# Kernel tuning notes

Measured on AMD Instinct MI355X. Metric: run time of the kernel, lower is better.

## Reference

```python
import jax, jax.numpy as jnp
import numpy as np

B, N, C, H, NH, NC = 4, 2048, 256, 128, 8, 3  # batch, points, in_ch, hidden, heads, classes
DH = H // NH


def setup_inputs() -> dict:
    key = jax.random.key(0)
    ki = iter(jax.random.split(key, 48))
    def w(shape, s=0.05):
        return jax.random.normal(next(ki), shape, jnp.float32) * s
    z = lambda n: jnp.zeros((n,), jnp.float32)
    o = lambda n: jnp.ones((n,), jnp.float32)
    inp = dict(x=jax.random.normal(next(ki), (B, N, C), jnp.float32))
    inp.update(fuse_w1=w((H, C)), fuse_b1=z(H), fuse_w2=w((H, H)), fuse_b2=z(H))
    for l in range(2):
        inp[f'attn{l}_in_w'] = w((3 * H, H)); inp[f'attn{l}_in_b'] = z(3 * H)
        inp[f'attn{l}_out_w'] = w((H, H)); inp[f'attn{l}_out_b'] = z(H)
        inp[f'ffn{l}_w1'] = w((2 * H, H)); inp[f'ffn{l}_b1'] = z(2 * H)
        inp[f'ffn{l}_w2'] = w((H, 2 * H)); inp[f'ffn{l}_b2'] = z(H)
        inp[f'ln{2*l}_g'] = o(H); inp[f'ln{2*l}_b'] = z(H)
        inp[f'ln{2*l+1}_g'] = o(H); inp[f'ln{2*l+1}_b'] = z(H)
    inp.update(out_w1=w((H, H)), out_b1=z(H), out_w2=w((NC, H)), out_b2=z(NC))
    inp.update(det_w1=w((H // 2, H)), det_b1=z(H // 2), det_w2=w((1, H // 2)), det_b2=z(1))
    return inp


def _ln(x, g, b):
    m = jnp.mean(x, axis=-1, keepdims=True)
    v = jnp.mean((x - m) ** 2, axis=-1, keepdims=True)
    return (x - m) * jax.lax.rsqrt(v + 1e-5) * g + b


def _mha(x, in_w, in_b, out_w, out_b):
    # nn.MultiheadAttention (batch_first, self-attn), eval mode (no dropout)
    Bq, Nq, _ = x.shape
    qkv = x @ in_w.T + in_b                          # [B,N,3H]
    q, k, v = jnp.split(qkv, 3, axis=-1)
    q = q.reshape(Bq, Nq, NH, DH)
    k = k.reshape(Bq, Nq, NH, DH)
    v = v.reshape(Bq, Nq, NH, DH)
    s = jnp.einsum('bqhd,bkhd->bhqk', q, k) / jnp.sqrt(jnp.float32(DH))
    a = jax.nn.softmax(s, axis=-1)
    o = jnp.einsum('bhqk,bkhd->bqhd', a, v).reshape(Bq, Nq, H)
    return o @ out_w.T + out_b


def _forward(x, fuse_w1, fuse_b1, fuse_w2, fuse_b2,
             attn0_in_w, attn0_in_b, attn0_out_w, attn0_out_b,
             ffn0_w1, ffn0_b1, ffn0_w2, ffn0_b2, ln0_g, ln0_b, ln1_g, ln1_b,
             attn1_in_w, attn1_in_b, attn1_out_w, attn1_out_b,
             ffn1_w1, ffn1_b1, ffn1_w2, ffn1_b2, ln2_g, ln2_b, ln3_g, ln3_b,
             out_w1, out_b1, out_w2, out_b2, det_w1, det_b1, det_w2, det_b2):
    # feature_fusion (dropout = identity in eval)
    h = jnp.maximum(x @ fuse_w1.T + fuse_b1, 0) @ fuse_w2.T + fuse_b2
    layers = [
        (attn0_in_w, attn0_in_b, attn0_out_w, attn0_out_b, ffn0_w1, ffn0_b1, ffn0_w2, ffn0_b2, ln0_g, ln0_b, ln1_g, ln1_b),
        (attn1_in_w, attn1_in_b, attn1_out_w, attn1_out_b, ffn1_w1, ffn1_b1, ffn1_w2, ffn1_b2, ln2_g, ln2_b, ln3_g, ln3_b),
    ]
    for (iw, ib, ow, ob, f1w, f1b, f2w, f2b, g1, be1, g2, be2) in layers:
        h = _ln(h + _mha(h, iw, ib, ow, ob), g1, be1)
        h = _ln(h + (jnp.maximum(h @ f1w.T + f1b, 0) @ f2w.T + f2b), g2, be2)
    refined_logits = jnp.maximum(h @ out_w1.T + out_b1, 0) @ out_w2.T + out_b2   # [B,N,NC]
    head_prob = jax.nn.sigmoid(jnp.maximum(h @ det_w1.T + det_b1, 0) @ det_w2.T + det_b2)[..., 0]  # [B,N]
    quality = jnp.mean(head_prob, axis=1)                                        # [B]
    return refined_logits, head_prob, quality


def reference(x, fuse_w1, fuse_b1, fuse_w2, fuse_b2,
              attn0_in_w, attn0_in_b, attn0_out_w, attn0_out_b,
              ffn0_w1, ffn0_b1, ffn0_w2, ffn0_b2, ln0_g, ln0_b, ln1_g, ln1_b,
              attn1_in_w, attn1_in_b, attn1_out_w, attn1_out_b,
              ffn1_w1, ffn1_b1, ffn1_w2, ffn1_b2, ln2_g, ln2_b, ln3_g, ln3_b,
              out_w1, out_b1, out_w2, out_b2, det_w1, det_b1, det_w2, det_b2):
    return _forward(x, fuse_w1, fuse_b1, fuse_w2, fuse_b2,
                    attn0_in_w, attn0_in_b, attn0_out_w, attn0_out_b,
                    ffn0_w1, ffn0_b1, ffn0_w2, ffn0_b2, ln0_g, ln0_b, ln1_g, ln1_b,
                    attn1_in_w, attn1_in_b, attn1_out_w, attn1_out_b,
                    ffn1_w1, ffn1_b1, ffn1_w2, ffn1_b2, ln2_g, ln2_b, ln3_g, ln3_b,
                    out_w1, out_b1, out_w2, out_b2, det_w1, det_b1, det_w2, det_b2)
```

## Files before the change

### kernel.cpp

```cpp
#include <hip/hip_runtime.h>
#include <cstddef>

constexpr int Bb  = 4;
constexpr int Nn  = 2048;
constexpr int Cc  = 256;
constexpr int Hh  = 128;
constexpr int NHh = 8;
constexpr int DHh = 16;
constexpr int MTOK = Bb * Nn;
#define LOG2E 1.4426950408889634f

typedef __attribute__((ext_vector_type(8))) short bf16x8;
typedef __attribute__((ext_vector_type(4))) short bf16x4;
typedef __attribute__((ext_vector_type(4))) float f32x4;

__device__ __forceinline__ short f32_to_bf16_rne(float f) {
    union { float f; unsigned int u; } c; c.f = f;
    unsigned int r = c.u + 0x7fffu + ((c.u >> 16) & 1u);
    return (short)(r >> 16);
}
__device__ __forceinline__ float bf16_to_f32(short s) {
    union { float f; unsigned int u; } c; c.u = ((unsigned int)(unsigned short)s) << 16;
    return c.f;
}
__device__ __forceinline__ unsigned pack2_bf16(float a, float b) {
    unsigned r;
    asm("v_cvt_pk_bf16_f32 %0, %1, %2" : "=v"(r) : "v"(a), "v"(b));
    return r;
}

struct CvtJobs {
    const float* src[13];
    short*       dst[13];
    int          off[14];
    float*       qzero;
};

__global__ __launch_bounds__(256) void cvt_kernel(CvtJobs j) {
    const int gid = blockIdx.x * 256 + threadIdx.x;
    if (blockIdx.x == 0 && threadIdx.x < 4) j.qzero[threadIdx.x] = 0.f;
    if (gid >= j.off[13]) return;
    int k = 0;
    #pragma unroll
    for (int i = 0; i < 12; ++i) if (gid >= j.off[i + 1]) k = i + 1;
    const int idx = (gid - j.off[k]) * 4;
    float4 v = *(const float4*)(j.src[k] + idx);
    short o4[4] = { f32_to_bf16_rne(v.x), f32_to_bf16_rne(v.y),
                    f32_to_bf16_rne(v.z), f32_to_bf16_rne(v.w) };
    *(bf16x4*)(j.dst[k] + idx) = *(bf16x4*)o4;
}

__global__ __launch_bounds__(256) void qkv_gemm_kernel(
    const short* __restrict__ X, const short* __restrict__ W,
    const float* __restrict__ bias, short* __restrict__ Yb)
{
    constexpr int K = 128, N = 384, ST = K + 8;
    __shared__ short As[64 * ST];
    __shared__ short Bs[64 * ST];

    const int tid  = threadIdx.x;
    const int lane = tid & 63;
    const int wv   = tid >> 6;
    const int col  = lane & 15;
    const int g    = lane >> 4;
    const int m0   = blockIdx.y * 64;
    const int n0   = blockIdx.x * 64;

    for (int i = tid; i < 64 * (K / 8); i += 256) {
        const int r = i / (K / 8), c = (i % (K / 8)) * 8;
        *(bf16x8*)&As[r * ST + c] = *(const bf16x8*)(X + (size_t)(m0 + r) * K + c);
        *(bf16x8*)&Bs[r * ST + c] = *(const bf16x8*)(W + (size_t)(n0 + r) * K + c);
    }
    __syncthreads();

    f32x4 acc[4] = {};
    #pragma unroll
    for (int k0 = 0; k0 < K; k0 += 32) {
        bf16x8 a = *(bf16x8*)&As[(wv * 16 + col) * ST + k0 + g * 8];
        #pragma unroll
        for (int jj = 0; jj < 4; ++jj) {
            bf16x8 b = *(bf16x8*)&Bs[(jj * 16 + col) * ST + k0 + g * 8];
            acc[jj] = __builtin_amdgcn_mfma_f32_16x16x32_bf16(a, b, acc[jj], 0, 0, 0);
        }
    }

    #pragma unroll
    for (int jj = 0; jj < 4; ++jj) {
        const int cn = n0 + jj * 16 + col;
        const float bb = bias[cn];
        #pragma unroll
        for (int r = 0; r < 4; ++r) {
            const int rm = m0 + wv * 16 + g * 4 + r;
            Yb[(size_t)rm * N + cn] = f32_to_bf16_rne(acc[jj][r] + bb);
        }
    }
}

__global__ __launch_bounds__(256) void postattn_kernel(
    const short* __restrict__ X,
    const short* __restrict__ Wo, const float* __restrict__ bo,
    const short* __restrict__ W1, const float* __restrict__ b1,
    const short* __restrict__ W2, const float* __restrict__ b2,
    float* __restrict__ hf, short* __restrict__ hb,
    const float* __restrict__ g1w, const float* __restrict__ b1w,
    const float* __restrict__ g2w, const float* __restrict__ b2w)
{
    __shared__ short As[16 * 136];
    __shared__ short Ws[64 * 136];
    __shared__ short U1[16 * 136];
    __shared__ short U2[16 * 264];
    float* P = (float*)Ws;

    const int tid  = threadIdx.x;
    const int lane = tid & 63;
    const int wv   = tid >> 6;
    const int col  = lane & 15;
    const int g    = lane >> 4;
    const int m0   = blockIdx.x * 16;
    const int cb   = wv * 16;

    bf16x8 wreg[4];
    auto loadPanel = [&](const short* base, int stride) {
        #pragma unroll
        for (int j = 0; j < 4; ++j) {
            const int i = tid + j * 256;
            wreg[j] = *(const bf16x8*)(base + (size_t)(i / 16) * stride + (i % 16) * 8);
        }
    };
    auto writePanel = [&]() {
        #pragma unroll
        for (int j = 0; j < 4; ++j) {
            const int i = tid + j * 256;
            *(bf16x8*)&Ws[(i / 16) * 136 + (i % 16) * 8] = wreg[j];
        }
    };

    {
        const int r = tid / 16, c = (tid % 16) * 8;
        *(bf16x8*)&As[r * 136 + c] = *(const bf16x8*)(X + (size_t)(m0 + r) * 128 + c);
    }
    loadPanel(Wo, 128);

    f32x4 ya[2] = {};
    #pragma unroll
    for (int ch = 0; ch < 2; ++ch) {
        writePanel();
        if (ch == 0) loadPanel(Wo + (size_t)64 * 128, 128);
        else         loadPanel(W1, 128);
        asm volatile("s_waitcnt lgkmcnt(0)" ::: "memory");
        __builtin_amdgcn_s_barrier();
        #pragma unroll
        for (int k0 = 0; k0 < 128; k0 += 32) {
            bf16x8 a = *(bf16x8*)&As[col * 136 + k0 + g * 8];
            bf16x8 b = *(bf16x8*)&Ws[(cb + col) * 136 + k0 + g * 8];
            ya[ch] = __builtin_amdgcn_mfma_f32_16x16x32_bf16(a, b, ya[ch], 0, 0, 0);
        }
        __syncthreads();
    }

    #pragma unroll
    for (int ch = 0; ch < 2; ++ch) {
        const int cn = ch * 64 + cb + col;
        const float bb = bo[cn];
        #pragma unroll
        for (int r = 0; r < 4; ++r)
            P[(g * 4 + r) * 130 + cn] = ya[ch][r] + bb;
    }
    __syncthreads();

    float2 resid[4];
    #pragma unroll
    for (int rr = 0; rr < 4; ++rr) {
        const int row = wv * 4 + rr;
        const size_t t = m0 + row;
        float2 pv = *(float2*)&P[row * 130 + 2 * lane];
        float2 hv = ((const float2*)(hf + t * Hh))[lane];
        float a0 = hv.x + pv.x, a1 = hv.y + pv.y;
        float sum = a0 + a1;
        #pragma unroll
        for (int off = 32; off > 0; off >>= 1) sum += __shfl_xor(sum, off);
        const float mean = sum * (1.f / 128.f);
        const float d0 = a0 - mean, d1 = a1 - mean;
        float vs = d0 * d0 + d1 * d1;
        #pragma unroll
        for (int off = 32; off > 0; off >>= 1) vs += __shfl_xor(vs, off);
        const float rstd = rsqrtf(vs * (1.f / 128.f) + 1e-5f);
        float2 gv = ((const float2*)g1w)[lane];
        float2 bv = ((const float2*)b1w)[lane];
        float2 r = { d0 * rstd * gv.x + bv.x, d1 * rstd * gv.y + bv.y };
        resid[rr] = r;
        *(unsigned*)&U1[row * 136 + 2 * lane] = pack2_bf16(r.x, r.y);
    }
    __syncthreads();

    #pragma unroll
    for (int ch = 0; ch < 4; ++ch) {
        writePanel();
        if (ch < 3) loadPanel(W1 + (size_t)(ch + 1) * 64 * 128, 128);
        else        loadPanel(W2, 256);
        asm volatile("s_waitcnt lgkmcnt(0)" ::: "memory");
        __builtin_amdgcn_s_barrier();
        f32x4 y1 = {};
        #pragma unroll
        for (int k0 = 0; k0 < 128; k0 += 32) {
            bf16x8 a = *(bf16x8*)&U1[col * 136 + k0 + g * 8];
            bf16x8 b = *(bf16x8*)&Ws[(cb + col) * 136 + k0 + g * 8];
            y1 = __builtin_amdgcn_mfma_f32_16x16x32_bf16(a, b, y1, 0, 0, 0);
        }
        __syncthreads();
        const int cn = ch * 64 + cb + col;
        const float bb = b1[cn];
        #pragma unroll
        for (int r = 0; r < 4; ++r)
            U2[(g * 4 + r) * 264 + cn] = f32_to_bf16_rne(fmaxf(y1[r] + bb, 0.f));
    }

    f32x4 yb[2] = {};
    #pragma unroll
    for (int ch2 = 0; ch2 < 2; ++ch2) {
        #pragma unroll
        for (int kh = 0; kh < 2; ++kh) {
            writePanel();
            const int pidx = ch2 * 2 + kh;
            if (pidx < 3) {
                const int nj = pidx + 1;
                loadPanel(W2 + (size_t)(nj >> 1) * 64 * 256 + (nj & 1) * 128, 256);
            }
            asm volatile("s_waitcnt lgkmcnt(0)" ::: "memory");
            __builtin_amdgcn_s_barrier();
            #pragma unroll
            for (int k0 = 0; k0 < 128; k0 += 32) {
                bf16x8 a = *(bf16x8*)&U2[col * 264 + kh * 128 + k0 + g * 8];
                bf16x8 b = *(bf16x8*)&Ws[(cb + col) * 136 + k0 + g * 8];
                yb[ch2] = __builtin_amdgcn_mfma_f32_16x16x32_bf16(a, b, yb[ch2], 0, 0, 0);
            }
            __syncthreads();
        }
    }

    #pragma unroll
    for (int ch2 = 0; ch2 < 2; ++ch2) {
        const int cn = ch2 * 64 + cb + col;
        const float bb = b2[cn];
        #pragma unroll
        for (int r = 0; r < 4; ++r)
            P[(g * 4 + r) * 130 + cn] = yb[ch2][r] + bb;
    }
    __syncthreads();

    #pragma unroll
    for (int rr = 0; rr < 4; ++rr) {
        const int row = wv * 4 + rr;
        const size_t t = m0 + row;
        float2 pv = *(float2*)&P[row * 130 + 2 * lane];
        float a0 = resid[rr].x + pv.x, a1 = resid[rr].y + pv.y;
        float sum = a0 + a1;
        #pragma unroll
        for (int off = 32; off > 0; off >>= 1) sum += __shfl_xor(sum, off);
        const float mean = sum * (1.f / 128.f);
        const float d0 = a0 - mean, d1 = a1 - mean;
        float vs = d0 * d0 + d1 * d1;
        #pragma unroll
        for (int off = 32; off > 0; off >>= 1) vs += __shfl_xor(vs, off);
        const float rstd = rsqrtf(vs * (1.f / 128.f) + 1e-5f);
        float2 gv = ((const float2*)g2w)[lane];
        float2 bv = ((const float2*)b2w)[lane];
        float2 r = { d0 * rstd * gv.x + bv.x, d1 * rstd * gv.y + bv.y };
        ((float2*)(hf + t * Hh))[lane] = r;
        *(unsigned*)&hb[t * Hh + lane * 2] = pack2_bf16(r.x, r.y);
    }
}

template<int K, int MID, bool DO_LN>
__global__ __launch_bounds__(256) void mlp2_kernel(
    const short* __restrict__ X,
    const short* __restrict__ W1, const float* __restrict__ b1,
    const short* __restrict__ W2, const float* __restrict__ b2,
    float* __restrict__ hf, short* __restrict__ hb,
    const float* __restrict__ gw, const float* __restrict__ bw)
{
    constexpr int STA = K + 8;
    constexpr int STU = MID + 8;
    constexpr int KP1  = K / 128;
    constexpr int KP2  = MID / 128;
    constexpr int NCH1 = MID / 64;
    constexpr int NP1  = NCH1 * KP1;
    constexpr int NP   = NP1 + 2 * KP2;
    __shared__ short As[16 * STA];
    __shared__ short Ws[64 * 136];
    __shared__ short U[16 * STU];
    float* P = (float*)Ws;

    const int tid  = threadIdx.x;
    const int lane = tid & 63;
    const int wv   = tid >> 6;
    const int col  = lane & 15;
    const int g    = lane >> 4;
    const int m0   = blockIdx.x * 16;
    const int cb   = wv * 16;

    bf16x8 wreg[4];
    auto loadPanelIdx = [&](int idx) {
        const short* base;
        int stride;
        if (idx < NP1) {
            const int ch = idx / KP1, kh = idx % KP1;
            base = W1 + (size_t)(ch * 64) * K + kh * 128; stride = K;
        } else {
            const int jj = idx - NP1;
            const int ch2 = jj / KP2, kh = jj % KP2;
            base = W2 + (size_t)(ch2 * 64) * MID + kh * 128; stride = MID;
        }
        #pragma unroll
        for (int j = 0; j < 4; ++j) {
            const int i = tid + j * 256;
            wreg[j] = *(const bf16x8*)(base + (size_t)(i / 16) * stride + (i % 16) * 8);
        }
    };
    auto writePanel = [&]() {
        #pragma unroll
        for (int j = 0; j < 4; ++j) {
            const int i = tid + j * 256;
            *(bf16x8*)&Ws[(i / 16) * 136 + (i % 16) * 8] = wreg[j];
        }
    };

    for (int i = tid; i < 16 * (K / 8); i += 256) {
        const int r = i / (K / 8), c = (i % (K / 8)) * 8;
        *(bf16x8*)&As[r * STA + c] = *(const bf16x8*)(X + (size_t)(m0 + r) * K + c);
    }
    loadPanelIdx(0);
    int pidx = 0;

    #pragma unroll
    for (int ch = 0; ch < NCH1; ++ch) {
        f32x4 ya = {};
        #pragma unroll
        for (int kh = 0; kh < KP1; ++kh) {
            writePanel();
            ++pidx;
            if (pidx < NP) loadPanelIdx(pidx);
            asm volatile("s_waitcnt lgkmcnt(0)" ::: "memory");
            __builtin_amdgcn_s_barrier();
            #pragma unroll
            for (int k0 = 0; k0 < 128; k0 += 32) {
                bf16x8 a = *(bf16x8*)&As[col * STA + kh * 128 + k0 + g * 8];
                bf16x8 b = *(bf16x8*)&Ws[(cb + col) * 136 + k0 + g * 8];
                ya = __builtin_amdgcn_mfma_f32_16x16x32_bf16(a, b, ya, 0, 0, 0);
            }
            __syncthreads();
        }
        const int cn = ch * 64 + cb + col;
        const float bb = b1[cn];
        #pragma unroll
        for (int r = 0; r < 4; ++r)
            U[(g * 4 + r) * STU + cn] = f32_to_bf16_rne(fmaxf(ya[r] + bb, 0.f));
    }

    f32x4 yb[2] = {};
    #pragma unroll
    for (int ch2 = 0; ch2 < 2; ++ch2) {
        #pragma unroll
        for (int kh = 0; kh < KP2; ++kh) {
            writePanel();
            ++pidx;
            if (pidx < NP) loadPanelIdx(pidx);
            asm volatile("s_waitcnt lgkmcnt(0)" ::: "memory");
            __builtin_amdgcn_s_barrier();
            #pragma unroll
            for (int k0 = 0; k0 < 128; k0 += 32) {
                bf16x8 a = *(bf16x8*)&U[col * STU + kh * 128 + k0 + g * 8];
                bf16x8 b = *(bf16x8*)&Ws[(cb + col) * 136 + k0 + g * 8];
                yb[ch2] = __builtin_amdgcn_mfma_f32_16x16x32_bf16(a, b, yb[ch2], 0, 0, 0);
            }
            __syncthreads();
        }
    }

    #pragma unroll
    for (int ch2 = 0; ch2 < 2; ++ch2) {
        const int cn = ch2 * 64 + cb + col;
        const float bb = b2[cn];
        #pragma unroll
        for (int r = 0; r < 4; ++r)
            P[(g * 4 + r) * 130 + cn] = yb[ch2][r] + bb;
    }
    __syncthreads();

    #pragma unroll
    for (int rr = 0; rr < 4; ++rr) {
        const int row = wv * 4 + rr;
        const size_t t = m0 + row;
        float2 pv = *(float2*)&P[row * 130 + 2 * lane];
        if (DO_LN) {
            float2 hv = ((const float2*)(hf + t * Hh))[lane];
            float a0 = hv.x + pv.x, a1 = hv.y + pv.y;
            float sum = a0 + a1;
            #pragma unroll
            for (int off = 32; off > 0; off >>= 1) sum += __shfl_xor(sum, off);
            const float mean = sum * (1.f / 128.f);
            const float d0 = a0 - mean, d1 = a1 - mean;
            float vs = d0 * d0 + d1 * d1;
            #pragma unroll
            for (int off = 32; off > 0; off >>= 1) vs += __shfl_xor(vs, off);
            const float rstd = rsqrtf(vs * (1.f / 128.f) + 1e-5f);
            float2 gv = ((const float2*)gw)[lane];
            float2 bv = ((const float2*)bw)[lane];
            float2 r = { d0 * rstd * gv.x + bv.x, d1 * rstd * gv.y + bv.y };
            ((float2*)(hf + t * Hh))[lane] = r;
            *(unsigned*)&hb[t * Hh + lane * 2] = pack2_bf16(r.x, r.y);
        } else {
            ((float2*)(hf + t * Hh))[lane] = pv;
            *(unsigned*)&hb[t * Hh + lane * 2] = pack2_bf16(pv.x, pv.y);
        }
    }
}

__global__ __launch_bounds__(256) void head_kernel(
    const short* __restrict__ X,
    const short* __restrict__ W1b, const float* __restrict__ b1,
    const short* __restrict__ DW1b, const float* __restrict__ db1,
    const float* __restrict__ w2, const float* __restrict__ b2,
    const float* __restrict__ dw2, const float* __restrict__ db2,
    float* __restrict__ out)
{
    constexpr int K = 128, ST = K + 8;
    __shared__ short As[32 * ST];
    __shared__ short Ws[64 * ST];
    __shared__ float P[32 * 196];

    const int tid  = threadIdx.x;
    const int lane = tid & 63;
    const int wv   = tid >> 6;
    const int col  = lane & 15;
    const int g    = lane >> 4;
    const int m0   = blockIdx.x * 32;
    const int mst  = (wv & 1) * 16;
    const int cb   = (wv >> 1) * 32;

    bf16x8 wreg[4];
    auto loadPanel = [&](const short* base) {
        #pragma unroll
        for (int j = 0; j < 4; ++j) {
            const int i = tid + j * 256;
            wreg[j] = *(const bf16x8*)(base + (size_t)(i / 16) * K + (i % 16) * 8);
        }
    };
    auto writePanel = [&]() {
        #pragma unroll
        for (int j = 0; j < 4; ++j) {
            const int i = tid + j * 256;
            *(bf16x8*)&Ws[(i / 16) * ST + (i % 16) * 8] = wreg[j];
        }
    };

    for (int i = tid; i < 32 * (K / 8); i += 256) {
        const int r = i / (K / 8), c = (i % (K / 8)) * 8;
        *(bf16x8*)&As[r * ST + c] = *(const bf16x8*)(X + (size_t)(m0 + r) * K + c);
    }
    loadPanel(W1b);

    f32x4 ya[3][2] = {};
    #pragma unroll
    for (int ch = 0; ch < 3; ++ch) {
        writePanel();
        if (ch == 0) loadPanel(W1b + (size_t)64 * K);
        else if (ch == 1) loadPanel(DW1b);
        asm volatile("s_waitcnt lgkmcnt(0)" ::: "memory");
        __builtin_amdgcn_s_barrier();
        #pragma unroll
        for (int k0 = 0; k0 < K; k0 += 32) {
            bf16x8 a = *(bf16x8*)&As[(mst + col) * ST + k0 + g * 8];
            #pragma unroll
            for (int f = 0; f < 2; ++f) {
                bf16x8 b = *(bf16x8*)&Ws[(cb + f * 16 + col) * ST + k0 + g * 8];
                ya[ch][f] = __builtin_amdgcn_mfma_f32_16x16x32_bf16(a, b, ya[ch][f], 0, 0, 0);
            }
        }
        __syncthreads();
    }

    #pragma unroll
    for (int ch = 0; ch < 3; ++ch)
        #pragma unroll
        for (int f = 0; f < 2; ++f) {
            const int cn = ch * 64 + cb + f * 16 + col;
            const float bb = (cn < 128) ? b1[cn] : db1[cn - 128];
            #pragma unroll
            for (int r = 0; r < 4; ++r)
                P[(mst + g * 4 + r) * 196 + cn] = fmaxf(ya[ch][f][r] + bb, 0.f);
        }
    __syncthreads();

    const float w20 = w2[2 * lane],       w21 = w2[2 * lane + 1];
    const float w22 = w2[128 + 2 * lane], w23 = w2[129 + 2 * lane];
    const float w24 = w2[256 + 2 * lane], w25 = w2[257 + 2 * lane];
    const float dwl = dw2[lane];
    float qacc = 0.f;
    #pragma unroll
    for (int rr = 0; rr < 8; ++rr) {
        const int row = wv * 8 + rr;
        const size_t t = m0 + row;
        const float x0 = P[row * 196 + 2 * lane];
        const float x1 = P[row * 196 + 2 * lane + 1];
        float s0 = x0 * w20 + x1 * w21;
        float s1 = x0 * w22 + x1 * w23;
        float s2 = x0 * w24 + x1 * w25;
        float d  = P[row * 196 + 128 + lane] * dwl;
        #pragma unroll
        for (int off = 32; off > 0; off >>= 1) {
            s0 += __shfl_xor(s0, off);
            s1 += __shfl_xor(s1, off);
            s2 += __shfl_xor(s2, off);
            d  += __shfl_xor(d,  off);
        }
        if (lane == 0) {
            out[t * 3 + 0] = s0 + b2[0];
            out[t * 3 + 1] = s1 + b2[1];
            out[t * 3 + 2] = s2 + b2[2];
            const float prob = 1.f / (1.f + __expf(-(d + db2[0])));
            out[24576 + t] = prob;
            qacc += prob;
        }
    }
    if (lane == 0)
        atomicAdd(&out[32768 + (m0 >> 11)], qacc * (1.f / (float)Nn));
}

constexpr int KT = 128;
constexpr int KS = 28;
constexpr int VS = 132;

__global__ __launch_bounds__(256) void attn_kernel(
    const short* __restrict__ qkv, short* __restrict__ out)
{
    __shared__ short Ks[KT * KS];
    __shared__ short Vs[DHh * VS];

    const int tid  = threadIdx.x;
    const int lane = tid & 63;
    const int wv   = tid >> 6;
    const int col  = lane & 15;
    const int g    = lane >> 4;
    const int hd   = blockIdx.y;
    const int b    = blockIdx.z;
    const int q0   = blockIdx.x * 64 + wv * 16;

    const short* base = qkv + (size_t)b * Nn * 384;

    bf16x8 qf = {};
    if (g < 2) {
        bf16x8 qraw = *(const bf16x8*)(base + (size_t)(q0 + col) * 384 + hd * DHh + g * 8);
        const float qs = 0.25f * LOG2E;
        #pragma unroll
        for (int i = 0; i < 8; ++i)
            qf[i] = f32_to_bf16_rne(bf16_to_f32(qraw[i]) * qs);
    }

    f32x4 o    = {0.f, 0.f, 0.f, 0.f};
    f32x4 lacc = {0.f, 0.f, 0.f, 0.f};
    const short one_bf16 = (short)0x3F80;
    const bf16x8 ones = { one_bf16, one_bf16, one_bf16, one_bf16,
                          one_bf16, one_bf16, one_bf16, one_bf16 };

    const int ksr = tid >> 1;
    const int ksd = (tid & 1) * 8;
    const int va  = tid >> 2;
    const int vd  = (tid & 3) * 4;

    const short* kptr = base + (size_t)ksr * 384 + Hh + hd * DHh + ksd;
    const short* vptr = base + (size_t)(2 * va) * 384 + 2 * Hh + hd * DHh + vd;
    bf16x8 kreg = *(const bf16x8*)kptr;
    bf16x4 vr0  = *(const bf16x4*)vptr;
    bf16x4 vr1  = *(const bf16x4*)(vptr + 384);

    for (int kt = 0; kt < Nn; kt += KT) {
        __syncthreads();

        *(bf16x8*)&Ks[ksr * KS + ksd] = kreg;
        {
            unsigned a0 = ((const unsigned*)&vr0)[0], a1 = ((const unsigned*)&vr0)[1];
            unsigned b0 = ((const unsigned*)&vr1)[0], b1 = ((const unsigned*)&vr1)[1];
            *(unsigned*)&Vs[(vd + 0) * VS + 2 * va] = __builtin_amdgcn_perm(b0, a0, 0x05040100);
            *(unsigned*)&Vs[(vd + 1) * VS + 2 * va] = __builtin_amdgcn_perm(b0, a0, 0x07060302);
            *(unsigned*)&Vs[(vd + 2) * VS + 2 * va] = __builtin_amdgcn_perm(b1, a1, 0x05040100);
            *(unsigned*)&Vs[(vd + 3) * VS + 2 * va] = __builtin_amdgcn_perm(b1, a1, 0x07060302);
        }

        if (kt + KT < Nn) {
            kptr += KT * 384;
            vptr += KT * 384;
            kreg = *(const bf16x8*)kptr;
            vr0  = *(const bf16x4*)vptr;
            vr1  = *(const bf16x4*)(vptr + 384);
        }

        asm volatile("s_waitcnt lgkmcnt(0)" ::: "memory");
        __builtin_amdgcn_s_barrier();

        __builtin_amdgcn_s_setprio(1);
        #pragma unroll
        for (int s = 0; s < 4; ++s) {
            bf16x8 kf0 = {}, kf1 = {};
            if (g < 2) {
                kf0 = *(bf16x8*)&Ks[(s * 32 + col) * KS + g * 8];
                kf1 = *(bf16x8*)&Ks[(s * 32 + 16 + col) * KS + g * 8];
            }
            f32x4 z = {0.f, 0.f, 0.f, 0.f};
            f32x4 sA = __builtin_amdgcn_mfma_f32_16x16x32_bf16(kf0, qf, z, 0, 0, 0);
            f32x4 sB = __builtin_amdgcn_mfma_f32_16x16x32_bf16(kf1, qf, z, 0, 0, 0);

            union { bf16x8 v; unsigned u[4]; } pf;
            pf.u[0] = pack2_bf16(__builtin_amdgcn_exp2f(sA[0]),
                                 __builtin_amdgcn_exp2f(sA[1]));
            pf.u[1] = pack2_bf16(__builtin_amdgcn_exp2f(sA[2]),
                                 __builtin_amdgcn_exp2f(sA[3]));
            pf.u[2] = pack2_bf16(__builtin_amdgcn_exp2f(sB[0]),
                                 __builtin_amdgcn_exp2f(sB[1]));
            pf.u[3] = pack2_bf16(__builtin_amdgcn_exp2f(sB[2]),
                                 __builtin_amdgcn_exp2f(sB[3]));

            bf16x8 vf;
            ((bf16x4*)&vf)[0] = *(bf16x4*)&Vs[col * VS + s * 32 + g * 4];
            ((bf16x4*)&vf)[1] = *(bf16x4*)&Vs[col * VS + s * 32 + 16 + g * 4];

            o    = __builtin_amdgcn_mfma_f32_16x16x32_bf16(pf.v, vf,   o,    0, 0, 0);
            lacc = __builtin_amdgcn_mfma_f32_16x16x32_bf16(pf.v, ones, lacc, 0, 0, 0);
        }
        __builtin_amdgcn_s_setprio(0);
    }

    #pragma unroll
    for (int r = 0; r < 4; ++r) {
        const float inv = __builtin_amdgcn_rcpf(lacc[r]);
        out[(size_t)(b * Nn + q0 + g * 4 + r) * Hh + hd * DHh + col] =
            f32_to_bf16_rne(o[r] * inv);
    }
}

extern "C" void kernel_launch(void* const* d_in, const int* in_sizes, int n_in,
                              void* d_out, int out_size, void* d_ws, size_t ws_size,
                              hipStream_t stream)
{
    char* W8 = (char*)d_ws;
    float* hf   = (float*)(W8 + 0);
    short* hb   = (short*)(W8 + 4194304);
    short* wb   = (short*)(W8 + 6291456);
    char*  regA = W8 + 7340032;
    char*  regB = W8 + 13631488;

    short* xb    = (short*)regA;
    short* qkvb  = (short*)regA;
    short* attno = (short*)regB;
    float* out   = (float*)d_out;

    const int wsz[12]  = {32768,16384,49152,16384,32768,32768,49152,16384,32768,32768,16384,8192};
    const int wsrc[12] = {1, 3, 5, 7, 9, 11, 17, 19, 21, 23, 29, 33};
    int woff[13]; woff[0] = 0;
    for (int i = 0; i < 12; ++i) woff[i + 1] = woff[i] + wsz[i];

    CvtJobs jobs;
    int acc = 0;
    for (int i = 0; i < 12; ++i) {
        jobs.src[i] = (const float*)d_in[wsrc[i]];
        jobs.dst[i] = wb + woff[i];
        jobs.off[i] = acc;
        acc += wsz[i] / 4;
    }
    jobs.src[12] = (const float*)d_in[0];
    jobs.dst[12] = xb;
    jobs.off[12] = acc;
    acc += (MTOK * Cc) / 4;
    jobs.off[13] = acc;
    jobs.qzero = out + 32768;

    hipLaunchKernelGGL(cvt_kernel, dim3((acc + 255) / 256), dim3(256), 0, stream, jobs);

    hipLaunchKernelGGL((mlp2_kernel<256, 128, false>), dim3(MTOK / 16), dim3(256), 0,
                       stream, xb, wb + woff[0], (const float*)d_in[2],
                       wb + woff[1], (const float*)d_in[4], hf, hb, nullptr, nullptr);

    for (int l = 0; l < 2; ++l) {
        const int ib = 5 + l * 12;
        const int wbase = 2 + l * 4;
        hipLaunchKernelGGL(qkv_gemm_kernel, dim3(384 / 64, MTOK / 64), dim3(256), 0, stream,
                           hb, wb + woff[wbase + 0], (const float*)d_in[ib + 1], qkvb);
        hipLaunchKernelGGL(attn_kernel, dim3(Nn / 64, NHh, Bb), dim3(256), 0, stream,
                           qkvb, attno);
        hipLaunchKernelGGL(postattn_kernel, dim3(MTOK / 16), dim3(256), 0, stream,
                           attno, wb + woff[wbase + 1], (const float*)d_in[ib + 3],
                           wb + woff[wbase + 2], (const float*)d_in[ib + 5],
                           wb + woff[wbase + 3], (const float*)d_in[ib + 7],
                           hf, hb,
                           (const float*)d_in[ib + 8], (const float*)d_in[ib + 9],
                           (const float*)d_in[ib + 10], (const float*)d_in[ib + 11]);
    }

    hipLaunchKernelGGL(head_kernel, dim3(MTOK / 32), dim3(256), 0, stream,
                       hb, wb + woff[10], (const float*)d_in[30],
                       wb + woff[11], (const float*)d_in[34],
                       (const float*)d_in[31], (const float*)d_in[32],
                       (const float*)d_in[35], (const float*)d_in[36], out);
}
```

Before: 254.5 us.

## Double-buffer LDS weight and K/V tiles to drop one barrier per stage

Weight panels in postattn and mlp2 and the K/V tiles in attention now alternate between two LDS buffers. That lets each loop iteration drop its trailing __syncthreads and keep only the single barrier after the write. sched_barrier calls are added to stop the compiler moving LDS reads across that barrier. This doubles LDS use for these buffers, which may lower occupancy, and correctness now relies on the single-barrier ping-pong ordering, including reuse of Ws[0] as the P scratch.

```diff
diff --git a/kernel.cpp b/kernel.cpp
--- a/kernel.cpp
+++ b/kernel.cpp
@@ -105,11 +105,11 @@
     const float* __restrict__ g1w, const float* __restrict__ b1w,
     const float* __restrict__ g2w, const float* __restrict__ b2w)
 {
+    __shared__ short Ws[2][64 * 136];
     __shared__ short As[16 * 136];
-    __shared__ short Ws[64 * 136];
     __shared__ short U1[16 * 136];
     __shared__ short U2[16 * 264];
-    float* P = (float*)Ws;
+    float* P = (float*)Ws[0];
 
     const int tid  = threadIdx.x;
     const int lane = tid & 63;
@@ -127,11 +127,11 @@
             wreg[j] = *(const bf16x8*)(base + (size_t)(i / 16) * stride + (i % 16) * 8);
         }
     };
-    auto writePanel = [&]() {
+    auto writePanel = [&](short* dst) {
         #pragma unroll
         for (int j = 0; j < 4; ++j) {
             const int i = tid + j * 256;
-            *(bf16x8*)&Ws[(i / 16) * 136 + (i % 16) * 8] = wreg[j];
+            *(bf16x8*)&dst[(i / 16) * 136 + (i % 16) * 8] = wreg[j];
         }
     };
 
@@ -144,18 +144,19 @@
     f32x4 ya[2] = {};
     #pragma unroll
     for (int ch = 0; ch < 2; ++ch) {
-        writePanel();
+        short* wb_ = Ws[ch & 1];
+        writePanel(wb_);
         if (ch == 0) loadPanel(Wo + (size_t)64 * 128, 128);
         else         loadPanel(W1, 128);
         asm volatile("s_waitcnt lgkmcnt(0)" ::: "memory");
         __builtin_amdgcn_s_barrier();
+        __builtin_amdgcn_sched_barrier(0);
         #pragma unroll
         for (int k0 = 0; k0 < 128; k0 += 32) {
             bf16x8 a = *(bf16x8*)&As[col * 136 + k0 + g * 8];
-            bf16x8 b = *(bf16x8*)&Ws[(cb + col) * 136 + k0 + g * 8];
+            bf16x8 b = *(bf16x8*)&wb_[(cb + col) * 136 + k0 + g * 8];
             ya[ch] = __builtin_amdgcn_mfma_f32_16x16x32_bf16(a, b, ya[ch], 0, 0, 0);
         }
-        __syncthreads();
     }
 
     #pragma unroll
@@ -195,19 +196,20 @@
 
     #pragma unroll
     for (int ch = 0; ch < 4; ++ch) {
-        writePanel();
+        short* wb_ = Ws[ch & 1];
+        writePanel(wb_);
         if (ch < 3) loadPanel(W1 + (size_t)(ch + 1) * 64 * 128, 128);
         else        loadPanel(W2, 256);
         asm volatile("s_waitcnt lgkmcnt(0)" ::: "memory");
         __builtin_amdgcn_s_barrier();
+        __builtin_amdgcn_sched_barrier(0);
         f32x4 y1 = {};
         #pragma unroll
         for (int k0 = 0; k0 < 128; k0 += 32) {
             bf16x8 a = *(bf16x8*)&U1[col * 136 + k0 + g * 8];
-            bf16x8 b = *(bf16x8*)&Ws[(cb + col) * 136 + k0 + g * 8];
+            bf16x8 b = *(bf16x8*)&wb_[(cb + col) * 136 + k0 + g * 8];
             y1 = __builtin_amdgcn_mfma_f32_16x16x32_bf16(a, b, y1, 0, 0, 0);
         }
-        __syncthreads();
         const int cn = ch * 64 + cb + col;
         const float bb = b1[cn];
         #pragma unroll
@@ -220,21 +222,22 @@
     for (int ch2 = 0; ch2 < 2; ++ch2) {
         #pragma unroll
         for (int kh = 0; kh < 2; ++kh) {
-            writePanel();
-            const int pidx = ch2 * 2 + kh;
-            if (pidx < 3) {
-                const int nj = pidx + 1;
+            const int j = ch2 * 2 + kh;
+            short* wb_ = Ws[j & 1];
+            writePanel(wb_);
+            if (j < 3) {
+                const int nj = j + 1;
                 loadPanel(W2 + (size_t)(nj >> 1) * 64 * 256 + (nj & 1) * 128, 256);
             }
             asm volatile("s_waitcnt lgkmcnt(0)" ::: "memory");
             __builtin_amdgcn_s_barrier();
+            __builtin_amdgcn_sched_barrier(0);
             #pragma unroll
             for (int k0 = 0; k0 < 128; k0 += 32) {
                 bf16x8 a = *(bf16x8*)&U2[col * 264 + kh * 128 + k0 + g * 8];
-                bf16x8 b = *(bf16x8*)&Ws[(cb + col) * 136 + k0 + g * 8];
+                bf16x8 b = *(bf16x8*)&wb_[(cb + col) * 136 + k0 + g * 8];
                 yb[ch2] = __builtin_amdgcn_mfma_f32_16x16x32_bf16(a, b, yb[ch2], 0, 0, 0);
             }
-            __syncthreads();
         }
     }
 
@@ -286,10 +289,10 @@
     constexpr int NCH1 = MID / 64;
     constexpr int NP1  = NCH1 * KP1;
     constexpr int NP   = NP1 + 2 * KP2;
+    __shared__ short Ws[2][64 * 136];
     __shared__ short As[16 * STA];
-    __shared__ short Ws[64 * 136];
     __shared__ short U[16 * STU];
-    float* P = (float*)Ws;
+    float* P = (float*)Ws[0];
 
     const int tid  = threadIdx.x;
     const int lane = tid & 63;
@@ -317,11 +320,11 @@
             wreg[j] = *(const bf16x8*)(base + (size_t)(i / 16) * stride + (i % 16) * 8);
         }
     };
-    auto writePanel = [&]() {
+    auto writePanel = [&](short* dst) {
         #pragma unroll
         for (int j = 0; j < 4; ++j) {
             const int i = tid + j * 256;
-            *(bf16x8*)&Ws[(i / 16) * 136 + (i % 16) * 8] = wreg[j];
+            *(bf16x8*)&dst[(i / 16) * 136 + (i % 16) * 8] = wreg[j];
         }
     };
 
@@ -337,18 +340,19 @@
         f32x4 ya = {};
         #pragma unroll
         for (int kh = 0; kh < KP1; ++kh) {
-            writePanel();
+            short* wb_ = Ws[pidx & 1];
+            writePanel(wb_);
+            if (pidx + 1 < NP) loadPanelIdx(pidx + 1);
             ++pidx;
-            if (pidx < NP) loadPanelIdx(pidx);
             asm volatile("s_waitcnt lgkmcnt(0)" ::: "memory");
             __builtin_amdgcn_s_barrier();
+            __builtin_amdgcn_sched_barrier(0);
             #pragma unroll
             for (int k0 = 0; k0 < 128; k0 += 32) {
                 bf16x8 a = *(bf16x8*)&As[col * STA + kh * 128 + k0 + g * 8];
-                bf16x8 b = *(bf16x8*)&Ws[(cb + col) * 136 + k0 + g * 8];
+                bf16x8 b = *(bf16x8*)&wb_[(cb + col) * 136 + k0 + g * 8];
                 ya = __builtin_amdgcn_mfma_f32_16x16x32_bf16(a, b, ya, 0, 0, 0);
             }
-            __syncthreads();
         }
         const int cn = ch * 64 + cb + col;
         const float bb = b1[cn];
@@ -362,18 +366,19 @@
     for (int ch2 = 0; ch2 < 2; ++ch2) {
         #pragma unroll
         for (int kh = 0; kh < KP2; ++kh) {
-            writePanel();
+            short* wb_ = Ws[pidx & 1];
+            writePanel(wb_);
+            if (pidx + 1 < NP) loadPanelIdx(pidx + 1);
             ++pidx;
-            if (pidx < NP) loadPanelIdx(pidx);
             asm volatile("s_waitcnt lgkmcnt(0)" ::: "memory");
             __builtin_amdgcn_s_barrier();
+            __builtin_amdgcn_sched_barrier(0);
             #pragma unroll
             for (int k0 = 0; k0 < 128; k0 += 32) {
                 bf16x8 a = *(bf16x8*)&U[col * STU + kh * 128 + k0 + g * 8];
-                bf16x8 b = *(bf16x8*)&Ws[(cb + col) * 136 + k0 + g * 8];
+                bf16x8 b = *(bf16x8*)&wb_[(cb + col) * 136 + k0 + g * 8];
                 yb[ch2] = __builtin_amdgcn_mfma_f32_16x16x32_bf16(a, b, yb[ch2], 0, 0, 0);
             }
-            __syncthreads();
         }
     }
 
@@ -468,6 +473,7 @@
         else if (ch == 1) loadPanel(DW1b);
         asm volatile("s_waitcnt lgkmcnt(0)" ::: "memory");
         __builtin_amdgcn_s_barrier();
+        __builtin_amdgcn_sched_barrier(0);
         #pragma unroll
         for (int k0 = 0; k0 < K; k0 += 32) {
             bf16x8 a = *(bf16x8*)&As[(mst + col) * ST + k0 + g * 8];
@@ -534,8 +540,8 @@
 __global__ __launch_bounds__(256) void attn_kernel(
     const short* __restrict__ qkv, short* __restrict__ out)
 {
-    __shared__ short Ks[KT * KS];
-    __shared__ short Vs[DHh * VS];
+    __shared__ short Ks[2][KT * KS];
+    __shared__ short Vs[2][DHh * VS];
 
     const int tid  = threadIdx.x;
     const int lane = tid & 63;
@@ -574,20 +580,21 @@
     bf16x4 vr0  = *(const bf16x4*)vptr;
     bf16x4 vr1  = *(const bf16x4*)(vptr + 384);
 
-    for (int kt = 0; kt < Nn; kt += KT) {
-        __syncthreads();
-
-        *(bf16x8*)&Ks[ksr * KS + ksd] = kreg;
+    for (int t = 0; t < Nn / KT; ++t) {
+        short* ks = Ks[t & 1];
+        short* vs = Vs[t & 1];
+
+        *(bf16x8*)&ks[ksr * KS + ksd] = kreg;
         {
             unsigned a0 = ((const unsigned*)&vr0)[0], a1 = ((const unsigned*)&vr0)[1];
             unsigned b0 = ((const unsigned*)&vr1)[0], b1 = ((const unsigned*)&vr1)[1];
-            *(unsigned*)&Vs[(vd + 0) * VS + 2 * va] = __builtin_amdgcn_perm(b0, a0, 0x05040100);
-            *(unsigned*)&Vs[(vd + 1) * VS + 2 * va] = __builtin_amdgcn_perm(b0, a0, 0x07060302);
-            *(unsigned*)&Vs[(vd + 2) * VS + 2 * va] = __builtin_amdgcn_perm(b1, a1, 0x05040100);
-            *(unsigned*)&Vs[(vd + 3) * VS + 2 * va] = __builtin_amdgcn_perm(b1, a1, 0x07060302);
-        }
-
-        if (kt + KT < Nn) {
+            *(unsigned*)&vs[(vd + 0) * VS + 2 * va] = __builtin_amdgcn_perm(b0, a0, 0x05040100);
+            *(unsigned*)&vs[(vd + 1) * VS + 2 * va] = __builtin_amdgcn_perm(b0, a0, 0x07060302);
+            *(unsigned*)&vs[(vd + 2) * VS + 2 * va] = __builtin_amdgcn_perm(b1, a1, 0x05040100);
+            *(unsigned*)&vs[(vd + 3) * VS + 2 * va] = __builtin_amdgcn_perm(b1, a1, 0x07060302);
+        }
+
+        if (t + 1 < Nn / KT) {
             kptr += KT * 384;
             vptr += KT * 384;
             kreg = *(const bf16x8*)kptr;
@@ -597,14 +604,15 @@
 
         asm volatile("s_waitcnt lgkmcnt(0)" ::: "memory");
         __builtin_amdgcn_s_barrier();
+        __builtin_amdgcn_sched_barrier(0);
 
         __builtin_amdgcn_s_setprio(1);
         #pragma unroll
         for (int s = 0; s < 4; ++s) {
             bf16x8 kf0 = {}, kf1 = {};
             if (g < 2) {
-                kf0 = *(bf16x8*)&Ks[(s * 32 + col) * KS + g * 8];
-                kf1 = *(bf16x8*)&Ks[(s * 32 + 16 + col) * KS + g * 8];
+                kf0 = *(bf16x8*)&ks[(s * 32 + col) * KS + g * 8];
+                kf1 = *(bf16x8*)&ks[(s * 32 + 16 + col) * KS + g * 8];
             }
             f32x4 z = {0.f, 0.f, 0.f, 0.f};
             f32x4 sA = __builtin_amdgcn_mfma_f32_16x16x32_bf16(kf0, qf, z, 0, 0, 0);
@@ -621,8 +629,8 @@
                                  __builtin_amdgcn_exp2f(sB[3]));
 
             bf16x8 vf;
-            ((bf16x4*)&vf)[0] = *(bf16x4*)&Vs[col * VS + s * 32 + g * 4];
-            ((bf16x4*)&vf)[1] = *(bf16x4*)&Vs[col * VS + s * 32 + 16 + g * 4];
+            ((bf16x4*)&vf)[0] = *(bf16x4*)&vs[col * VS + s * 32 + g * 4];
+            ((bf16x4*)&vf)[1] = *(bf16x4*)&vs[col * VS + s * 32 + 16 + g * 4];
 
             o    = __builtin_amdgcn_mfma_f32_16x16x32_bf16(pf.v, vf,   o,    0, 0, 0);
             lacc = __builtin_amdgcn_mfma_f32_16x16x32_bf16(pf.v, ones, lacc, 0, 0, 0);
```

After: 287.9 us. +13.1%, slower.
